# Optimization experiments

Hardware: AMD Instinct MI355X
Metric: run time of the kernel (lower is better)

The kernel has to match this reference:

```python
import jax, jax.numpy as jnp
import numpy as np

HEADS = 4  # from init_kwargs

def _branch_index(seq_len: int) -> jnp.ndarray:
    # position 0 -> layer_s(0), 1 -> layer_r(1), 2 -> layer_o(2),
    # then alternating layer_a(3)/layer_v(4) starting at position 3.
    tail = jnp.where((jnp.arange(seq_len - 3) % 2) == 0, 3, 4)
    return jnp.concatenate([jnp.array([0, 1, 2], dtype=tail.dtype), tail])


def setup_inputs() -> dict:
    key = jax.random.key(0)
    k1, k2, k3 = jax.random.split(key, 3)
    B, S, H = 128, 513, 256
    x = jax.random.normal(k1, (B, S, H), dtype=jnp.float32)
    # 5 Linear layers, nn.Linear convention: y = x @ W.T + b, W: [out,in]
    W = jax.random.normal(k2, (5, H, H), dtype=jnp.float32) * (1.0 / np.sqrt(H))
    b = jax.random.normal(k3, (5, H), dtype=jnp.float32) * 0.02
    return {"x": x, "W": W, "b": b}


def reference(x, W, b):
    # Original applies each Linear to a position-masked copy of x and sums.
    # Since the 5 masks are disjoint one-hots over positions, the weight term
    # at position t is x[t] @ W[m(t)].T; the bias term is sum of ALL 5 biases
    # (Linear(0) = bias), applied at every position.
    B, S, H = x.shape
    idx = _branch_index(S)            # [S] in {0..4}
    Wsel = W[idx]
    out = jnp.einsum('bsh,sdh->bsd', x, Wsel) + b.sum(axis=0)
    return out.reshape(B, S, HEADS, H // HEADS)
```

## Files before the change

kernel.cpp:

```cpp
#include <hip/hip_runtime.h>
#include <hip/hip_bf16.h>

#define B_ 128
#define S_ 513
#define H_ 256
#define SH_ (S_ * H_)

typedef __attribute__((ext_vector_type(8))) short short8;
typedef __attribute__((ext_vector_type(4))) float f32x4;

static __device__ inline short8 pack8(float4 a, float4 b) {
    union { short8 s; __hip_bfloat162 h[4]; } u;
    u.h[0] = __float22bfloat162_rn(make_float2(a.x, a.y));
    u.h[1] = __float22bfloat162_rn(make_float2(a.z, a.w));
    u.h[2] = __float22bfloat162_rn(make_float2(b.x, b.y));
    u.h[3] = __float22bfloat162_rn(make_float2(b.z, b.w));
    return u.s;
}

static __device__ inline unsigned short f2bf(float f) {
    union { float f; unsigned int u; } v; v.f = f;
    unsigned int u = v.u;
    unsigned int r = u + 0x7fffu + ((u >> 16) & 1u);
    return (unsigned short)(r >> 16);
}

__global__ void prep_kernel(const float* __restrict__ W,
                            const float* __restrict__ bias,
                            unsigned short* __restrict__ Wbf,
                            float* __restrict__ bsum) {
    int t = blockIdx.x * 256 + threadIdx.x;
    if (t < 5 * H_ * H_ / 4) {
        float4 v = *(const float4*)(W + (size_t)t * 4);
        ushort4 p;
        p.x = f2bf(v.x); p.y = f2bf(v.y); p.z = f2bf(v.z); p.w = f2bf(v.w);
        *(ushort4*)(Wbf + (size_t)t * 4) = p;
    }
    if (t < H_) {
        float s = 0.f;
#pragma unroll
        for (int i = 0; i < 5; ++i) s += bias[i * H_ + t];
        bsum[t] = s;
    }
}

template <int MODE>
__global__ __launch_bounds__(512, 2)
void sel_gemm_kernel(const float* __restrict__ x,
                     const void* __restrict__ Wp,
                     const void* __restrict__ bp,
                     float* __restrict__ out) {
    const int s = blockIdx.x;
    const int m_idx = (s < 3) ? s : ((s & 1) ? 3 : 4);

    __shared__ unsigned short As[128 * 256];

    const int t    = threadIdx.x;
    const int lane = t & 63;
    const int w    = t >> 6;
    const int wn   = w & 3;
    const int wm   = w >> 1 >> 1;
    const int lrow = lane & 15;
    const int quad = lane >> 4;

    short8 bfr[4][8];
    if (MODE == 0) {
        const unsigned short* Wb =
            (const unsigned short*)Wp + (size_t)m_idx * H_ * H_;
#pragma unroll
        for (int j = 0; j < 4; ++j) {
            const unsigned short* wrow = Wb + (size_t)(wn * 64 + j * 16 + lrow) * H_;
#pragma unroll
            for (int kk = 0; kk < 8; ++kk)
                bfr[j][kk] = *(const short8*)(wrow + kk * 32 + quad * 8);
        }
    } else {
        const float* Wb = (const float*)Wp + (size_t)m_idx * H_ * H_;
#pragma unroll
        for (int j = 0; j < 4; ++j) {
            const float* wrow = Wb + (size_t)(wn * 64 + j * 16 + lrow) * H_;
#pragma unroll
            for (int kk = 0; kk < 8; ++kk) {
                float4 v0 = *(const float4*)(wrow + kk * 32 + quad * 8);
                float4 v1 = *(const float4*)(wrow + kk * 32 + quad * 8 + 4);
                bfr[j][kk] = pack8(v0, v1);
            }
        }
    }

    const float* xs = x + (size_t)s * H_;
#pragma unroll
    for (int i = 0; i < 8; ++i) {
        int flat = i * 512 + t;
        int r = flat >> 5;
        int c = flat & 31;
        const float* src = xs + (size_t)r * SH_ + c * 8;
        float4 v0 = *(const float4*)src;
        float4 v1 = *(const float4*)(src + 4);
        *(short8*)&As[r * 256 + ((c ^ (r & 7)) * 8)] = pack8(v0, v1);
    }

    f32x4 acc[4][4];
#pragma unroll
    for (int i = 0; i < 4; ++i)
#pragma unroll
        for (int j = 0; j < 4; ++j) {
            f32x4 z = {0.f, 0.f, 0.f, 0.f};
            acc[i][j] = z;
        }

    __syncthreads();

#pragma unroll
    for (int kk = 0; kk < 8; ++kk) {
        const int cc = kk * 4 + quad;
        short8 afr[4];
#pragma unroll
        for (int i = 0; i < 4; ++i) {
            int r = wm * 64 + i * 16 + lrow;
            afr[i] = *(const short8*)&As[r * 256 + ((cc ^ (r & 7)) * 8)];
        }
#pragma unroll
        for (int j = 0; j < 4; ++j)
#pragma unroll
            for (int i = 0; i < 4; ++i)
                acc[i][j] = __builtin_amdgcn_mfma_f32_16x16x32_bf16(
                    afr[i], bfr[j][kk], acc[i][j], 0, 0, 0);
    }

    float bs[4];
    if (MODE == 0) {
        const float* bsum = (const float*)bp;
#pragma unroll
        for (int j = 0; j < 4; ++j) bs[j] = bsum[wn * 64 + j * 16 + lrow];
    } else {
        const float* bias = (const float*)bp;
#pragma unroll
        for (int j = 0; j < 4; ++j) {
            int d = wn * 64 + j * 16 + lrow;
            float sum = 0.f;
#pragma unroll
            for (int i = 0; i < 5; ++i) sum += bias[i * H_ + d];
            bs[j] = sum;
        }
    }

#pragma unroll
    for (int i = 0; i < 4; ++i) {
#pragma unroll
        for (int r = 0; r < 4; ++r) {
            int bg = wm * 64 + i * 16 + quad * 4 + r;
            float* orow = out + ((size_t)bg * S_ + s) * H_;
#pragma unroll
            for (int j = 0; j < 4; ++j) {
                int d = wn * 64 + j * 16 + lrow;
                orow[d] = acc[i][j][r] + bs[j];
            }
        }
    }
}

extern "C" void kernel_launch(void* const* d_in, const int* in_sizes, int n_in,
                              void* d_out, int out_size, void* d_ws, size_t ws_size,
                              hipStream_t stream) {
    const float* x    = (const float*)d_in[0];
    const float* W    = (const float*)d_in[1];
    const float* bias = (const float*)d_in[2];
    float* out = (float*)d_out;

    const size_t w_elems  = (size_t)5 * H_ * H_;
    const size_t ws_need  = w_elems * sizeof(unsigned short) + H_ * sizeof(float);

    if (ws_size >= ws_need) {
        unsigned short* Wbf = (unsigned short*)d_ws;
        float* bsum = (float*)((char*)d_ws + w_elems * sizeof(unsigned short));
        prep_kernel<<<dim3((w_elems / 4 + 255) / 256), dim3(256), 0, stream>>>(
            W, bias, Wbf, bsum);
        sel_gemm_kernel<0><<<dim3(S_), dim3(512), 0, stream>>>(
            x, (const void*)Wbf, (const void*)bsum, out);
    } else {
        sel_gemm_kernel<1><<<dim3(S_), dim3(512), 0, stream>>>(
            x, (const void*)W, (const void*)bias, out);
    }
}
```

Before: 136.4 us.

## Split batch across blocks, pre-swizzle bf16 weights, swap MFMA operands for vector stores

Each sequence position is now handled by two 256-thread blocks, each covering half of the batch, which doubles the grid and halves LDS per block to raise occupancy. The prep kernel writes the bf16 weights in a k-chunk-major layout so that each wave's per-k fragment loads are contiguous. Weights are now streamed inside the k loop instead of being held in registers up front. Swapping the MFMA operands puts the output d dimension in the per-lane accumulator registers, so the epilogue can use float4 stores with a vector bias load. The cost is that weight traffic per position doubles because both halves reload the same W slice.

```diff
diff --git a/kernel.cpp b/kernel.cpp
--- a/kernel.cpp
+++ b/kernel.cpp
@@ -18,23 +18,20 @@
     return u.s;
 }
 
-static __device__ inline unsigned short f2bf(float f) {
-    union { float f; unsigned int u; } v; v.f = f;
-    unsigned int u = v.u;
-    unsigned int r = u + 0x7fffu + ((u >> 16) & 1u);
-    return (unsigned short)(r >> 16);
-}
-
 __global__ void prep_kernel(const float* __restrict__ W,
                             const float* __restrict__ bias,
                             unsigned short* __restrict__ Wbf,
                             float* __restrict__ bsum) {
     int t = blockIdx.x * 256 + threadIdx.x;
-    if (t < 5 * H_ * H_ / 4) {
-        float4 v = *(const float4*)(W + (size_t)t * 4);
-        ushort4 p;
-        p.x = f2bf(v.x); p.y = f2bf(v.y); p.z = f2bf(v.z); p.w = f2bf(v.w);
-        *(ushort4*)(Wbf + (size_t)t * 4) = p;
+    if (t < 5 * 32 * 256) {
+        int m  = t >> 13;
+        int r  = t & 8191;
+        int d  = r >> 5;
+        int kc = r & 31;
+        const float* src = W + (((size_t)m * 256 + d) * 256 + kc * 8);
+        float4 v0 = *(const float4*)src;
+        float4 v1 = *(const float4*)(src + 4);
+        *(short8*)(Wbf + ((size_t)(m * 32 + kc) * 256 + d) * 8) = pack8(v0, v1);
     }
     if (t < H_) {
         float s = 0.f;
@@ -45,53 +42,27 @@
 }
 
 template <int MODE>
-__global__ __launch_bounds__(512, 2)
+__global__ __launch_bounds__(256, 4)
 void sel_gemm_kernel(const float* __restrict__ x,
                      const void* __restrict__ Wp,
                      const void* __restrict__ bp,
                      float* __restrict__ out) {
-    const int s = blockIdx.x;
+    const int s     = blockIdx.x >> 1;
+    const int bhalf = blockIdx.x & 1;
     const int m_idx = (s < 3) ? s : ((s & 1) ? 3 : 4);
 
-    __shared__ unsigned short As[128 * 256];
+    __shared__ unsigned short As[64 * 256];
 
     const int t    = threadIdx.x;
     const int lane = t & 63;
     const int w    = t >> 6;
-    const int wn   = w & 3;
-    const int wm   = w >> 1 >> 1;
     const int lrow = lane & 15;
     const int quad = lane >> 4;
 
-    short8 bfr[4][8];
-    if (MODE == 0) {
-        const unsigned short* Wb =
-            (const unsigned short*)Wp + (size_t)m_idx * H_ * H_;
-#pragma unroll
-        for (int j = 0; j < 4; ++j) {
-            const unsigned short* wrow = Wb + (size_t)(wn * 64 + j * 16 + lrow) * H_;
-#pragma unroll
-            for (int kk = 0; kk < 8; ++kk)
-                bfr[j][kk] = *(const short8*)(wrow + kk * 32 + quad * 8);
-        }
-    } else {
-        const float* Wb = (const float*)Wp + (size_t)m_idx * H_ * H_;
-#pragma unroll
-        for (int j = 0; j < 4; ++j) {
-            const float* wrow = Wb + (size_t)(wn * 64 + j * 16 + lrow) * H_;
-#pragma unroll
-            for (int kk = 0; kk < 8; ++kk) {
-                float4 v0 = *(const float4*)(wrow + kk * 32 + quad * 8);
-                float4 v1 = *(const float4*)(wrow + kk * 32 + quad * 8 + 4);
-                bfr[j][kk] = pack8(v0, v1);
-            }
-        }
-    }
-
-    const float* xs = x + (size_t)s * H_;
+    const float* xs = x + (size_t)s * H_ + (size_t)bhalf * 64 * SH_;
 #pragma unroll
     for (int i = 0; i < 8; ++i) {
-        int flat = i * 512 + t;
+        int flat = i * 256 + t;
         int r = flat >> 5;
         int c = flat & 31;
         const float* src = xs + (size_t)r * SH_ + c * 8;
@@ -113,49 +84,63 @@
 
 #pragma unroll
     for (int kk = 0; kk < 8; ++kk) {
+        short8 wfr[4];
+        if (MODE == 0) {
+            const unsigned short* Wk =
+                (const unsigned short*)Wp +
+                ((size_t)(m_idx * 32 + kk * 4 + quad) * 256) * 8;
+#pragma unroll
+            for (int j = 0; j < 4; ++j)
+                wfr[j] = *(const short8*)(Wk + (size_t)(w * 64 + j * 16 + lrow) * 8);
+        } else {
+            const float* Wb = (const float*)Wp + (size_t)m_idx * H_ * H_;
+#pragma unroll
+            for (int j = 0; j < 4; ++j) {
+                const float* wrow = Wb + (size_t)(w * 64 + j * 16 + lrow) * H_
+                                    + kk * 32 + quad * 8;
+                float4 v0 = *(const float4*)wrow;
+                float4 v1 = *(const float4*)(wrow + 4);
+                wfr[j] = pack8(v0, v1);
+            }
+        }
+
+        short8 xfr[4];
         const int cc = kk * 4 + quad;
-        short8 afr[4];
 #pragma unroll
         for (int i = 0; i < 4; ++i) {
-            int r = wm * 64 + i * 16 + lrow;
-            afr[i] = *(const short8*)&As[r * 256 + ((cc ^ (r & 7)) * 8)];
+            int r = i * 16 + lrow;
+            xfr[i] = *(const short8*)&As[r * 256 + ((cc ^ (r & 7)) * 8)];
         }
+
 #pragma unroll
         for (int j = 0; j < 4; ++j)
 #pragma unroll
             for (int i = 0; i < 4; ++i)
                 acc[i][j] = __builtin_amdgcn_mfma_f32_16x16x32_bf16(
-                    afr[i], bfr[j][kk], acc[i][j], 0, 0, 0);
-    }
-
-    float bs[4];
-    if (MODE == 0) {
-        const float* bsum = (const float*)bp;
-#pragma unroll
-        for (int j = 0; j < 4; ++j) bs[j] = bsum[wn * 64 + j * 16 + lrow];
-    } else {
-        const float* bias = (const float*)bp;
-#pragma unroll
-        for (int j = 0; j < 4; ++j) {
-            int d = wn * 64 + j * 16 + lrow;
-            float sum = 0.f;
-#pragma unroll
-            for (int i = 0; i < 5; ++i) sum += bias[i * H_ + d];
-            bs[j] = sum;
-        }
+                    wfr[j], xfr[i], acc[i][j], 0, 0, 0);
     }
 
 #pragma unroll
-    for (int i = 0; i < 4; ++i) {
+    for (int j = 0; j < 4; ++j) {
+        const int d0 = w * 64 + j * 16 + quad * 4;
+        f32x4 bj;
+        if (MODE == 0) {
+            bj = *(const f32x4*)((const float*)bp + d0);
+        } else {
+            const float* bias = (const float*)bp;
 #pragma unroll
-        for (int r = 0; r < 4; ++r) {
-            int bg = wm * 64 + i * 16 + quad * 4 + r;
-            float* orow = out + ((size_t)bg * S_ + s) * H_;
+            for (int r = 0; r < 4; ++r) {
+                float sum = 0.f;
 #pragma unroll
-            for (int j = 0; j < 4; ++j) {
-                int d = wn * 64 + j * 16 + lrow;
-                orow[d] = acc[i][j][r] + bs[j];
+                for (int i = 0; i < 5; ++i) sum += bias[i * H_ + d0 + r];
+                bj[r] = sum;
             }
+        }
+#pragma unroll
+        for (int i = 0; i < 4; ++i) {
+            const int b = bhalf * 64 + i * 16 + lrow;
+            f32x4 v = acc[i][j] + bj;
+            *(f32x4*)(out + ((size_t)b * S_ + s) * H_ + d0) = v;
         }
     }
 }
@@ -174,12 +159,11 @@
     if (ws_size >= ws_need) {
         unsigned short* Wbf = (unsigned short*)d_ws;
         float* bsum = (float*)((char*)d_ws + w_elems * sizeof(unsigned short));
-        prep_kernel<<<dim3((w_elems / 4 + 255) / 256), dim3(256), 0, stream>>>(
-            W, bias, Wbf, bsum);
-        sel_gemm_kernel<0><<<dim3(S_), dim3(512), 0, stream>>>(
+        prep_kernel<<<dim3(160), dim3(256), 0, stream>>>(W, bias, Wbf, bsum);
+        sel_gemm_kernel<0><<<dim3(2 * S_), dim3(256), 0, stream>>>(
             x, (const void*)Wbf, (const void*)bsum, out);
     } else {
-        sel_gemm_kernel<1><<<dim3(S_), dim3(512), 0, stream>>>(
+        sel_gemm_kernel<1><<<dim3(2 * S_), dim3(256), 0, stream>>>(
             x, (const void*)W, (const void*)bias, out);
     }
 }
```

After: 130.9 us. -4.0%, faster.
